# Optimization experiments

Hardware: AMD Instinct MI355X
Metric: run time of the kernel (lower is better)

## Reference

```python
import jax, jax.numpy as jnp
import numpy as np

B, S, E = 2, 2048, 1024
H, D = 16, 64  # num_heads, head_dim


def setup_inputs() -> dict:
    key = jax.random.key(0)
    k1, k2, k3 = jax.random.split(key, 3)
    x = jax.random.normal(k1, (B, S, E), dtype=jnp.float32)
    # nnx normal() init has stddev 0.01; scale to keep magnitudes realistic
    w_qkv = jax.random.normal(k2, (E, H, 3 * D), dtype=jnp.float32) * 0.01
    w_out = jax.random.normal(k3, (H, D, E), dtype=jnp.float32) * 0.01
    return {"x": x, "w_qkv": w_qkv, "w_out": w_out}


def _attention(q, k, v):
    # q,k,v: [B, S, H, D]
    dtype = q.dtype
    logits = jnp.einsum('bqhd,bkhd->bhqk', q.astype(jnp.float32), k.astype(jnp.float32))
    logits = logits / jnp.sqrt(jnp.float32(q.shape[-1]))
    mask = jnp.tril(jnp.ones((q.shape[1], q.shape[1]), dtype=jnp.bool_))
    neg = jnp.asarray(-0.7 * jnp.finfo(logits.dtype).max, dtype=logits.dtype)
    logits = jnp.where(mask, logits, neg)
    probs = jax.nn.softmax(logits, axis=-1).astype(dtype)
    return jnp.einsum('bhqk,bkhd->bqhd', probs, v)


def reference(x, w_qkv, w_out):
    # qkv projection: [B,S,E] x [E,H,3D] -> [B,S,H,3D]
    qkv = jnp.einsum('bse,ehd->bshd', x, w_qkv)
    q, k, v = jnp.split(qkv, 3, axis=-1)
    out = _attention(q, k, v)  # [B,S,H,D]
    # output projection contracts (H,D) -> E
    return jnp.einsum('bshd,hde->bse', out, w_out)
```

## Files before the change

### kernel.cpp

```cpp
#include <hip/hip_runtime.h>

typedef unsigned short u16;
typedef unsigned int u32;
typedef __attribute__((ext_vector_type(8))) short bf16x8;
typedef __attribute__((ext_vector_type(4))) float f32x4;
typedef __attribute__((ext_vector_type(16))) float f32x16;
typedef __attribute__((ext_vector_type(4))) u32 u32x4;

#define MFMA16(a, b, c) __builtin_amdgcn_mfma_f32_16x16x32_bf16((a), (b), (c), 0, 0, 0)
#define MFMA32(a, b, c) __builtin_amdgcn_mfma_f32_32x32x16_bf16((a), (b), (c), 0, 0, 0)

__device__ __forceinline__ void async_lds16(void* lds, const void* g) {
  __builtin_amdgcn_global_load_lds(
      (const __attribute__((address_space(1))) void*)g,
      (__attribute__((address_space(3))) void*)lds, 16, 0, 0);
}

__device__ __forceinline__ u16 f2bf(float f) {
  union { float f; unsigned u; } v; v.f = f;
  unsigned r = v.u + 0x7fffu + ((v.u >> 16) & 1u);
  return (u16)(r >> 16);
}

__device__ __forceinline__ u32 cvt_pk_bf16(float lo, float hi) {
  u32 r;
  asm("v_cvt_pk_bf16_f32 %0, %1, %2" : "=v"(r) : "v"(lo), "v"(hi));
  return r;
}

__device__ __forceinline__ float exp2_fast(float x) {
  float r;
  asm("v_exp_f32 %0, %1" : "=v"(r) : "v"(x));
  return r;
}

__device__ __forceinline__ void pswap(u32& a, u32& b) {
  asm("v_permlane32_swap_b32 %0, %1" : "+v"(a), "+v"(b));
}


__global__ __launch_bounds__(256) void k_cvt(const float* __restrict__ in, u16* __restrict__ out, int n) {
  int i = (blockIdx.x * 256 + threadIdx.x) * 4;
  if (i >= n) return;
  float4 v = *(const float4*)(in + i);
  ushort4 o;
  o.x = f2bf(v.x); o.y = f2bf(v.y); o.z = f2bf(v.z); o.w = f2bf(v.w);
  *(ushort4*)(out + i) = o;
}

__global__ __launch_bounds__(256) void k_transpose_cvt(const float* __restrict__ in, u16* __restrict__ out,
                                                       int R, int C) {
  __shared__ float tile[32][33];
  int c0 = blockIdx.x * 32, r0 = blockIdx.y * 32;
  int tx = threadIdx.x & 31, ty = threadIdx.x >> 5;
#pragma unroll
  for (int i = 0; i < 32; i += 8)
    tile[ty + i][tx] = in[(long)(r0 + ty + i) * C + c0 + tx];
  __syncthreads();
#pragma unroll
  for (int i = 0; i < 32; i += 8)
    out[(long)(c0 + ty + i) * R + r0 + tx] = f2bf(tile[tx][ty + i]);
}

__global__ __launch_bounds__(256) void k_transpose_v(const u16* __restrict__ V, u16* __restrict__ Vt) {
  int bh = blockIdx.z;
  int s0 = blockIdx.x * 32, d0 = blockIdx.y * 32;
  __shared__ u16 tile[32][33];
  int tx = threadIdx.x & 31, ty = threadIdx.x >> 5;
  const u16* Vb = V + (long)bh * 2048 * 64;
  u16* Vtb = Vt + (long)bh * 64 * 2048;
#pragma unroll
  for (int i = 0; i < 32; i += 8)
    tile[ty + i][tx] = Vb[(long)(s0 + ty + i) * 64 + d0 + tx];
  __syncthreads();
#pragma unroll
  for (int i = 0; i < 32; i += 8)
    Vtb[(long)(d0 + ty + i) * 2048 + s0 + tx] = tile[tx][ty + i];
}


template <int BM, int BN, int NW, int WN, int MR, int NR>
__device__ __forceinline__ void gemm_core_pipe(const u16* __restrict__ A, const u16* __restrict__ Bt,
                                               int K, long row0, long col0,
                                               u16* sA, u16* sB, f32x4 (&acc)[MR][NR]) {
  const int NTHR = NW * 64;
  const int ABYTES = BM * 64 * 2;
  const int BBYTES = BN * 64 * 2;
  const int t = threadIdx.x;
  const int lane = t & 63, g = lane >> 4, m16 = lane & 15;
  const int wid = t >> 6, wr = wid / WN, wc = wid % WN;
  const int nkt = K >> 6;

  auto stage = [&](int buf, int kt) {
    const int k0 = kt << 6;
#pragma unroll
    for (int it = 0; it < ABYTES / (NTHR * 16); ++it) {
      int i = it * NTHR + t;
      int r = i >> 3, c = i & 7, cs = c ^ (r & 7);
      async_lds16((char*)sA + buf * ABYTES + i * 16, A + (row0 + r) * K + k0 + cs * 8);
    }
#pragma unroll
    for (int it = 0; it < BBYTES / (NTHR * 16); ++it) {
      int i = it * NTHR + t;
      int r = i >> 3, c = i & 7, cs = c ^ (r & 7);
      async_lds16((char*)sB + buf * BBYTES + i * 16, Bt + (col0 + r) * K + k0 + cs * 8);
    }
  };

  stage(0, 0);
  stage(1, 1);
  int cur = 0;
  for (int kt = 0; kt < nkt; ++kt) {
    if (kt + 1 < nkt) asm volatile("s_waitcnt vmcnt(8)" ::: "memory");
    else              asm volatile("s_waitcnt vmcnt(0)" ::: "memory");
    __builtin_amdgcn_s_barrier();
    __builtin_amdgcn_sched_barrier(0);
    const char* bA = (const char*)sA + cur * ABYTES;
    const char* bB = (const char*)sB + cur * BBYTES;
#pragma unroll
    for (int kk6 = 0; kk6 < 2; ++kk6) {
      const int ke = kk6 * 32 + 8 * g;
      bf16x8 av[MR], bv[NR];
#pragma unroll
      for (int mi = 0; mi < MR; ++mi) {
        int row = wr * (MR * 16) + mi * 16 + m16;
        av[mi] = *(const bf16x8*)(bA + (row << 7) + ((ke << 1) ^ ((row & 7) << 4)));
      }
#pragma unroll
      for (int ni = 0; ni < NR; ++ni) {
        int row = wc * (NR * 16) + ni * 16 + m16;
        bv[ni] = *(const bf16x8*)(bB + (row << 7) + ((ke << 1) ^ ((row & 7) << 4)));
      }
#pragma unroll
      for (int mi = 0; mi < MR; ++mi)
#pragma unroll
        for (int ni = 0; ni < NR; ++ni)
          acc[mi][ni] = MFMA16(av[mi], bv[ni], acc[mi][ni]);
    }
    __builtin_amdgcn_sched_barrier(0);
    __builtin_amdgcn_s_barrier();
    if (kt + 2 < nkt) stage(cur, kt + 2);
    cur ^= 1;
  }
}

__global__ __launch_bounds__(512, 2) void k_gemm_qkv(const u16* __restrict__ xb, const u16* __restrict__ wT,
                                                     u16* __restrict__ Qo, u16* __restrict__ Ko,
                                                     u16* __restrict__ Vo) {
  __shared__ __align__(16) u16 sA[2 * 256 * 64];
  __shared__ __align__(16) u16 sB[2 * 256 * 64];
  f32x4 acc[8][4];
  const f32x4 z = {0.f, 0.f, 0.f, 0.f};
#pragma unroll
  for (int mi = 0; mi < 8; ++mi)
#pragma unroll
    for (int ni = 0; ni < 4; ++ni) acc[mi][ni] = z;
  const int L = blockIdx.x;
  const int xcd = L & 7, idx = L >> 3;
  const int rowt = xcd * 2 + (idx & 1);
  const int colt = idx >> 1;
  long row0 = (long)rowt * 256, col0 = (long)colt * 256;
  gemm_core_pipe<256, 256, 8, 4, 8, 4>(xb, wT, 1024, row0, col0, sA, sB, acc);
  const int t = threadIdx.x;
  const int lane = t & 63, g = lane >> 4, m16 = lane & 15;
  const int wid = t >> 6, wr = wid >> 2, wc = wid & 3;
#pragma unroll
  for (int mi = 0; mi < 8; ++mi) {
#pragma unroll
    for (int ni = 0; ni < 4; ++ni) {
      int col = (int)col0 + wc * 64 + ni * 16 + m16;
      int h = col / 192, rem = col - h * 192;
      int which = rem >> 6, d = rem & 63;
#pragma unroll
      for (int r = 0; r < 4; ++r) {
        int row = (int)row0 + wr * 128 + mi * 16 + 4 * g + r;
        int b = row >> 11, s = row & 2047;
        long off = (((long)(b * 16 + h)) * 2048 + s) * 64 + d;
        float v = acc[mi][ni][r];
        if (which == 0) Qo[off] = f2bf(v * 0.18033688f);
        else if (which == 1) Ko[off] = f2bf(v);
        else Vo[off] = f2bf(v);
      }
    }
  }
}

__global__ __launch_bounds__(256) void k_gemm_out(const u16* __restrict__ Ob, const u16* __restrict__ wT,
                                                  float* __restrict__ out) {
  __shared__ __align__(16) u16 sA[2 * 128 * 64];
  __shared__ __align__(16) u16 sB[2 * 128 * 64];
  f32x4 acc[4][4];
  const f32x4 z = {0.f, 0.f, 0.f, 0.f};
#pragma unroll
  for (int mi = 0; mi < 4; ++mi)
#pragma unroll
    for (int ni = 0; ni < 4; ++ni) acc[mi][ni] = z;
  const int L = blockIdx.x;
  const int xcd = L & 7, idx = L >> 3;
  const int rowt = xcd * 4 + (idx & 3);
  const int colt = idx >> 2;
  long row0 = (long)rowt * 128, col0 = (long)colt * 128;
  gemm_core_pipe<128, 128, 4, 2, 4, 4>(Ob, wT, 1024, row0, col0, sA, sB, acc);
  const int t = threadIdx.x;
  const int lane = t & 63, g = lane >> 4, m16 = lane & 15;
  const int wid = t >> 6, wr = wid >> 1, wc = wid & 1;
#pragma unroll
  for (int mi = 0; mi < 4; ++mi) {
#pragma unroll
    for (int ni = 0; ni < 4; ++ni) {
#pragma unroll
      for (int r = 0; r < 4; ++r) {
        long row = row0 + wr * 64 + mi * 16 + 4 * g + r;
        long col = col0 + wc * 64 + ni * 16 + m16;
        out[row * 1024 + col] = acc[mi][ni][r];
      }
    }
  }
}


template <bool DIAG>
__device__ __forceinline__ void attn_sub(const char* Kt, const char* Vt, int bsub,
                                         bf16x8 qf0, bf16x8 qf1, bf16x8 qf2, bf16x8 qf3,
                                         f32x16& acc0, f32x16& acc1, float& l,
                                         int q5, int hi) {
  const int x7 = q5 & 7;
  const int rowK = (bsub * 32 + q5) << 7;
  bf16x8 k0 = *(const bf16x8*)(Kt + rowK + (((0 + hi) ^ x7) << 4));
  bf16x8 k1 = *(const bf16x8*)(Kt + rowK + (((2 + hi) ^ x7) << 4));
  bf16x8 k2 = *(const bf16x8*)(Kt + rowK + (((4 + hi) ^ x7) << 4));
  bf16x8 k3 = *(const bf16x8*)(Kt + rowK + (((6 + hi) ^ x7) << 4));
  const int rowV0 = q5 << 7, rowV1 = (q5 + 32) << 7;
  bf16x8 v00 = *(const bf16x8*)(Vt + rowV0 + (((bsub * 4 + 0 + hi) ^ x7) << 4));
  bf16x8 v01 = *(const bf16x8*)(Vt + rowV1 + (((bsub * 4 + 0 + hi) ^ x7) << 4));
  bf16x8 v10 = *(const bf16x8*)(Vt + rowV0 + (((bsub * 4 + 2 + hi) ^ x7) << 4));
  bf16x8 v11 = *(const bf16x8*)(Vt + rowV1 + (((bsub * 4 + 2 + hi) ^ x7) << 4));

  f32x16 s;
#pragma unroll
  for (int r = 0; r < 16; ++r) s[r] = 0.f;
  s = MFMA32(k0, qf0, s);
  s = MFMA32(k1, qf1, s);
  s = MFMA32(k2, qf2, s);
  s = MFMA32(k3, qf3, s);

  float p[16];
#pragma unroll
  for (int r = 0; r < 16; ++r) {
    float pv = exp2_fast(s[r]);
    if (DIAG) {
      int crow = (r & 3) + 8 * (r >> 2) + 4 * hi;
      pv = (crow <= q5) ? pv : 0.f;
    }
    p[r] = pv;
  }
  l += (((p[0] + p[1]) + (p[2] + p[3])) + ((p[4] + p[5]) + (p[6] + p[7]))) +
       (((p[8] + p[9]) + (p[10] + p[11])) + ((p[12] + p[13]) + (p[14] + p[15])));

  u32 a0 = cvt_pk_bf16(p[0], p[1]), a1 = cvt_pk_bf16(p[2], p[3]);
  u32 b0 = cvt_pk_bf16(p[4], p[5]), b1 = cvt_pk_bf16(p[6], p[7]);
  pswap(a0, b0); pswap(a1, b1);
  u32 c0 = cvt_pk_bf16(p[8], p[9]), c1 = cvt_pk_bf16(p[10], p[11]);
  u32 d0 = cvt_pk_bf16(p[12], p[13]), d1 = cvt_pk_bf16(p[14], p[15]);
  pswap(c0, d0); pswap(c1, d1);
  u32x4 t0; t0[0] = a0; t0[1] = a1; t0[2] = b0; t0[3] = b1;
  u32x4 t1; t1[0] = c0; t1[1] = c1; t1[2] = d0; t1[3] = d1;
  bf16x8 pa0 = __builtin_bit_cast(bf16x8, t0);
  bf16x8 pa1 = __builtin_bit_cast(bf16x8, t1);

  acc0 = MFMA32(pa0, v00, acc0);
  acc1 = MFMA32(pa0, v01, acc1);
  acc0 = MFMA32(pa1, v10, acc0);
  acc1 = MFMA32(pa1, v11, acc1);
}

__global__ __launch_bounds__(256) void k_attn(const u16* __restrict__ Qg, const u16* __restrict__ Kg,
                                              const u16* __restrict__ Vtg, u16* __restrict__ Og) {
  __shared__ __align__(16) u16 sK[2][64 * 64];
  __shared__ __align__(16) u16 sV[2][64 * 64];
  const int t = threadIdx.x;
  const int lane = t & 63, q5 = lane & 31, hi = lane >> 5, w = t >> 6;
  const int L = blockIdx.x;
  const int bh = L & 31, pr = L >> 5;
  const int qtA = pr, qtB = 15 - pr;
  const int b = bh >> 4, h = bh & 15;
  const u16* Qh = Qg + (long)bh * 131072;
  const u16* Kh = Kg + (long)bh * 131072;
  const u16* Vh = Vtg + (long)bh * 131072;
  char* sKb = (char*)sK;
  char* sVb = (char*)sV;

  const int sL_ = qtA * 4 + w, sH_ = qtB * 4 + w;
  const int q0L = sL_ * 32, q0H = sH_ * 32;
  const int nkt = 2 * qtB + 2;

  const u16* QpL = Qh + (long)(q0L + q5) * 64 + hi * 8;
  bf16x8 qfL0 = *(const bf16x8*)(QpL);
  bf16x8 qfL1 = *(const bf16x8*)(QpL + 16);
  bf16x8 qfL2 = *(const bf16x8*)(QpL + 32);
  bf16x8 qfL3 = *(const bf16x8*)(QpL + 48);
  const u16* QpH = Qh + (long)(q0H + q5) * 64 + hi * 8;
  bf16x8 qfH0 = *(const bf16x8*)(QpH);
  bf16x8 qfH1 = *(const bf16x8*)(QpH + 16);
  bf16x8 qfH2 = *(const bf16x8*)(QpH + 32);
  bf16x8 qfH3 = *(const bf16x8*)(QpH + 48);

  f32x16 aL0, aL1, aH0, aH1;
#pragma unroll
  for (int r = 0; r < 16; ++r) { aL0[r] = 0.f; aL1[r] = 0.f; aH0[r] = 0.f; aH1[r] = 0.f; }
  float lL = 0.f, lH = 0.f;

  auto stage = [&](int buf, int kt) {
    const int kbase = kt << 6;
#pragma unroll
    for (int ps = 0; ps < 2; ++ps) {
      int i = ps * 256 + t;
      int r = i >> 3, c = i & 7, cs = c ^ (r & 7);
      async_lds16(sKb + buf * 8192 + i * 16, Kh + (long)(kbase + r) * 64 + cs * 8);
    }
#pragma unroll
    for (int ps = 0; ps < 2; ++ps) {
      int i = ps * 256 + t;
      int d = i >> 3, c = i & 7, cs = c ^ (d & 7);
      async_lds16(sVb + buf * 8192 + i * 16, Vh + (long)d * 2048 + kbase + cs * 8);
    }
  };

  stage(0, 0);
  stage(1, 1);
  int cur = 0;
#pragma unroll 1
  for (int kt = 0; kt < nkt; ++kt) {
    if (kt + 1 < nkt) asm volatile("s_waitcnt vmcnt(4)" ::: "memory");
    else              asm volatile("s_waitcnt vmcnt(0)" ::: "memory");
    __builtin_amdgcn_s_barrier();
    __builtin_amdgcn_sched_barrier(0);
    const char* Kt = sKb + cur * 8192;
    const char* Vt = sVb + cur * 8192;
    const int c2 = 2 * kt;
    if (c2 <= sH_) {
      if (c2 == sH_) attn_sub<true>(Kt, Vt, 0, qfH0, qfH1, qfH2, qfH3, aH0, aH1, lH, q5, hi);
      else           attn_sub<false>(Kt, Vt, 0, qfH0, qfH1, qfH2, qfH3, aH0, aH1, lH, q5, hi);
    }
    if (c2 + 1 <= sH_) {
      if (c2 + 1 == sH_) attn_sub<true>(Kt, Vt, 1, qfH0, qfH1, qfH2, qfH3, aH0, aH1, lH, q5, hi);
      else               attn_sub<false>(Kt, Vt, 1, qfH0, qfH1, qfH2, qfH3, aH0, aH1, lH, q5, hi);
    }
    if (c2 <= sL_) {
      if (c2 == sL_) attn_sub<true>(Kt, Vt, 0, qfL0, qfL1, qfL2, qfL3, aL0, aL1, lL, q5, hi);
      else           attn_sub<false>(Kt, Vt, 0, qfL0, qfL1, qfL2, qfL3, aL0, aL1, lL, q5, hi);
    }
    if (c2 + 1 <= sL_) {
      if (c2 + 1 == sL_) attn_sub<true>(Kt, Vt, 1, qfL0, qfL1, qfL2, qfL3, aL0, aL1, lL, q5, hi);
      else               attn_sub<false>(Kt, Vt, 1, qfL0, qfL1, qfL2, qfL3, aL0, aL1, lL, q5, hi);
    }
    __builtin_amdgcn_sched_barrier(0);
    __builtin_amdgcn_s_barrier();
    if (kt + 2 < nkt) stage(cur, kt + 2);
    cur ^= 1;
  }

  const long orow_base = (long)b * 2048;
  lH += __shfl_xor(lH, 32);
  float liH = 1.0f / lH;
#pragma unroll
  for (int r = 0; r < 16; ++r) {
    int crow = (r & 3) + 8 * (r >> 2) + 4 * hi;
    float lf = __shfl(liH, crow);
    long orow = orow_base + q0H + crow;
    Og[orow * 1024 + h * 64 + q5] = f2bf(aH0[r] * lf);
    Og[orow * 1024 + h * 64 + 32 + q5] = f2bf(aH1[r] * lf);
  }
  lL += __shfl_xor(lL, 32);
  float liL = 1.0f / lL;
#pragma unroll
  for (int r = 0; r < 16; ++r) {
    int crow = (r & 3) + 8 * (r >> 2) + 4 * hi;
    float lf = __shfl(liL, crow);
    long orow = orow_base + q0L + crow;
    Og[orow * 1024 + h * 64 + q5] = f2bf(aL0[r] * lf);
    Og[orow * 1024 + h * 64 + 32 + q5] = f2bf(aL1[r] * lf);
  }
}


extern "C" void kernel_launch(void* const* d_in, const int* in_sizes, int n_in,
                              void* d_out, int out_size, void* d_ws, size_t ws_size,
                              hipStream_t stream) {
  const float* x = (const float*)d_in[0];
  const float* w_qkv = (const float*)d_in[1];
  const float* w_out = (const float*)d_in[2];
  float* out = (float*)d_out;
  char* ws = (char*)d_ws;

  u16* xb    = (u16*)(ws + 0);
  u16* wqkvT = (u16*)(ws + 8388608L);
  u16* woutT = (u16*)(ws + 14680064L);
  u16* Qb    = (u16*)(ws + 16777216L);
  u16* Kb    = (u16*)(ws + 25165824L);
  u16* Vb    = (u16*)(ws + 33554432L);
  u16* Vt    = (u16*)(ws + 41943040L);
  u16* Ob    = xb;

  k_cvt<<<4096, 256, 0, stream>>>(x, xb, 4194304);
  k_transpose_cvt<<<dim3(96, 32), 256, 0, stream>>>(w_qkv, wqkvT, 1024, 3072);
  k_transpose_cvt<<<dim3(32, 32), 256, 0, stream>>>(w_out, woutT, 1024, 1024);
  k_gemm_qkv<<<dim3(192), 512, 0, stream>>>(xb, wqkvT, Qb, Kb, Vb);
  k_transpose_v<<<dim3(64, 2, 32), 256, 0, stream>>>(Vb, Vt);
  k_attn<<<dim3(256), 256, 0, stream>>>(Qb, Kb, Vt, Ob);
  k_gemm_out<<<dim3(256), 256, 0, stream>>>(Ob, woutT, out);
}
```

Measured before the change: 122.5 us.

## Merge prep kernels, retile QKV GEMM to per-head 192 columns, raise MFMA priority

Three launches (x conversion and two weight transpose-converts) become one k_prep kernel that dispatches on block index, removing two launch gaps. The QKV GEMM tile changes from 256x256 to 256x192, so each column tile covers exactly one head, giving 256 blocks instead of 192 and simpler epilogue index math. The vmcnt wait is adjusted to the new load count. Attention MFMA sections are wrapped in s_setprio to favour the matrix issue; the smaller tile slightly lowers reuse per block.

Measured after the change: 113.3 us. -7.5%, faster.

```diff
diff --git a/kernel.cpp b/kernel.cpp
--- a/kernel.cpp
+++ b/kernel.cpp
@@ -39,19 +39,10 @@
 }
 
 
-__global__ __launch_bounds__(256) void k_cvt(const float* __restrict__ in, u16* __restrict__ out, int n) {
-  int i = (blockIdx.x * 256 + threadIdx.x) * 4;
-  if (i >= n) return;
-  float4 v = *(const float4*)(in + i);
-  ushort4 o;
-  o.x = f2bf(v.x); o.y = f2bf(v.y); o.z = f2bf(v.z); o.w = f2bf(v.w);
-  *(ushort4*)(out + i) = o;
-}
-
-__global__ __launch_bounds__(256) void k_transpose_cvt(const float* __restrict__ in, u16* __restrict__ out,
-                                                       int R, int C) {
-  __shared__ float tile[32][33];
-  int c0 = blockIdx.x * 32, r0 = blockIdx.y * 32;
+__device__ __forceinline__ void transpose_cvt_body(const float* __restrict__ in, u16* __restrict__ out,
+                                                   int R, int C, int bx, int by,
+                                                   float (*tile)[33]) {
+  int c0 = bx * 32, r0 = by * 32;
   int tx = threadIdx.x & 31, ty = threadIdx.x >> 5;
 #pragma unroll
   for (int i = 0; i < 32; i += 8)
@@ -60,6 +51,26 @@
 #pragma unroll
   for (int i = 0; i < 32; i += 8)
     out[(long)(c0 + ty + i) * R + r0 + tx] = f2bf(tile[tx][ty + i]);
+}
+
+__global__ __launch_bounds__(256) void k_prep(const float* __restrict__ x, u16* __restrict__ xb,
+                                              const float* __restrict__ w_qkv, u16* __restrict__ wqkvT,
+                                              const float* __restrict__ w_out, u16* __restrict__ woutT) {
+  __shared__ float tile[32][33];
+  const int B = blockIdx.x;
+  if (B < 4096) {
+    int i = (B * 256 + threadIdx.x) * 4;
+    float4 v = *(const float4*)(x + i);
+    ushort4 o;
+    o.x = f2bf(v.x); o.y = f2bf(v.y); o.z = f2bf(v.z); o.w = f2bf(v.w);
+    *(ushort4*)(xb + i) = o;
+  } else if (B < 7168) {
+    int bb = B - 4096;
+    transpose_cvt_body(w_qkv, wqkvT, 1024, 3072, bb % 96, bb / 96, tile);
+  } else {
+    int bb = B - 7168;
+    transpose_cvt_body(w_out, woutT, 1024, 1024, bb & 31, bb >> 5, tile);
+  }
 }
 
 __global__ __launch_bounds__(256) void k_transpose_v(const u16* __restrict__ V, u16* __restrict__ Vt) {
@@ -79,7 +90,7 @@
 }
 
 
-template <int BM, int BN, int NW, int WN, int MR, int NR>
+template <int BM, int BN, int NW, int WN, int WCS, int MR, int NR, int NLD>
 __device__ __forceinline__ void gemm_core_pipe(const u16* __restrict__ A, const u16* __restrict__ Bt,
                                                int K, long row0, long col0,
                                                u16* sA, u16* sB, f32x4 (&acc)[MR][NR]) {
@@ -111,8 +122,12 @@
   stage(1, 1);
   int cur = 0;
   for (int kt = 0; kt < nkt; ++kt) {
-    if (kt + 1 < nkt) asm volatile("s_waitcnt vmcnt(8)" ::: "memory");
-    else              asm volatile("s_waitcnt vmcnt(0)" ::: "memory");
+    if (kt + 1 < nkt) {
+      if constexpr (NLD == 7) asm volatile("s_waitcnt vmcnt(7)" ::: "memory");
+      else                    asm volatile("s_waitcnt vmcnt(8)" ::: "memory");
+    } else {
+      asm volatile("s_waitcnt vmcnt(0)" ::: "memory");
+    }
     __builtin_amdgcn_s_barrier();
     __builtin_amdgcn_sched_barrier(0);
     const char* bA = (const char*)sA + cur * ABYTES;
@@ -128,7 +143,7 @@
       }
 #pragma unroll
       for (int ni = 0; ni < NR; ++ni) {
-        int row = wc * (NR * 16) + ni * 16 + m16;
+        int row = wc * WCS + ni * 16 + m16;
         bv[ni] = *(const bf16x8*)(bB + (row << 7) + ((ke << 1) ^ ((row & 7) << 4)));
       }
 #pragma unroll
@@ -148,28 +163,28 @@
                                                      u16* __restrict__ Qo, u16* __restrict__ Ko,
                                                      u16* __restrict__ Vo) {
   __shared__ __align__(16) u16 sA[2 * 256 * 64];
-  __shared__ __align__(16) u16 sB[2 * 256 * 64];
-  f32x4 acc[8][4];
+  __shared__ __align__(16) u16 sB[2 * 192 * 64];
+  f32x4 acc[8][3];
   const f32x4 z = {0.f, 0.f, 0.f, 0.f};
 #pragma unroll
   for (int mi = 0; mi < 8; ++mi)
 #pragma unroll
-    for (int ni = 0; ni < 4; ++ni) acc[mi][ni] = z;
+    for (int ni = 0; ni < 3; ++ni) acc[mi][ni] = z;
   const int L = blockIdx.x;
   const int xcd = L & 7, idx = L >> 3;
   const int rowt = xcd * 2 + (idx & 1);
   const int colt = idx >> 1;
-  long row0 = (long)rowt * 256, col0 = (long)colt * 256;
-  gemm_core_pipe<256, 256, 8, 4, 8, 4>(xb, wT, 1024, row0, col0, sA, sB, acc);
+  long row0 = (long)rowt * 256, col0 = (long)colt * 192;
+  gemm_core_pipe<256, 192, 8, 4, 48, 8, 3, 7>(xb, wT, 1024, row0, col0, sA, sB, acc);
   const int t = threadIdx.x;
   const int lane = t & 63, g = lane >> 4, m16 = lane & 15;
   const int wid = t >> 6, wr = wid >> 2, wc = wid & 3;
+  const int h = colt;
 #pragma unroll
   for (int mi = 0; mi < 8; ++mi) {
 #pragma unroll
-    for (int ni = 0; ni < 4; ++ni) {
-      int col = (int)col0 + wc * 64 + ni * 16 + m16;
-      int h = col / 192, rem = col - h * 192;
+    for (int ni = 0; ni < 3; ++ni) {
+      int rem = wc * 48 + ni * 16 + m16;
       int which = rem >> 6, d = rem & 63;
 #pragma unroll
       for (int r = 0; r < 4; ++r) {
@@ -200,7 +215,7 @@
   const int rowt = xcd * 4 + (idx & 3);
   const int colt = idx >> 2;
   long row0 = (long)rowt * 128, col0 = (long)colt * 128;
-  gemm_core_pipe<128, 128, 4, 2, 4, 4>(Ob, wT, 1024, row0, col0, sA, sB, acc);
+  gemm_core_pipe<128, 128, 4, 2, 64, 4, 4, 8>(Ob, wT, 1024, row0, col0, sA, sB, acc);
   const int t = threadIdx.x;
   const int lane = t & 63, g = lane >> 4, m16 = lane & 15;
   const int wid = t >> 6, wr = wid >> 1, wc = wid & 1;
@@ -239,10 +254,12 @@
   f32x16 s;
 #pragma unroll
   for (int r = 0; r < 16; ++r) s[r] = 0.f;
+  __builtin_amdgcn_s_setprio(1);
   s = MFMA32(k0, qf0, s);
   s = MFMA32(k1, qf1, s);
   s = MFMA32(k2, qf2, s);
   s = MFMA32(k3, qf3, s);
+  __builtin_amdgcn_s_setprio(0);
 
   float p[16];
 #pragma unroll
@@ -268,10 +285,12 @@
   bf16x8 pa0 = __builtin_bit_cast(bf16x8, t0);
   bf16x8 pa1 = __builtin_bit_cast(bf16x8, t1);
 
+  __builtin_amdgcn_s_setprio(1);
   acc0 = MFMA32(pa0, v00, acc0);
   acc1 = MFMA32(pa0, v01, acc1);
   acc0 = MFMA32(pa1, v10, acc0);
   acc1 = MFMA32(pa1, v11, acc1);
+  __builtin_amdgcn_s_setprio(0);
 }
 
 __global__ __launch_bounds__(256) void k_attn(const u16* __restrict__ Qg, const u16* __restrict__ Kg,
@@ -402,10 +421,8 @@
   u16* Vt    = (u16*)(ws + 41943040L);
   u16* Ob    = xb;
 
-  k_cvt<<<4096, 256, 0, stream>>>(x, xb, 4194304);
-  k_transpose_cvt<<<dim3(96, 32), 256, 0, stream>>>(w_qkv, wqkvT, 1024, 3072);
-  k_transpose_cvt<<<dim3(32, 32), 256, 0, stream>>>(w_out, woutT, 1024, 1024);
-  k_gemm_qkv<<<dim3(192), 512, 0, stream>>>(xb, wqkvT, Qb, Kb, Vb);
+  k_prep<<<dim3(8192), 256, 0, stream>>>(x, xb, w_qkv, wqkvT, w_out, woutT);
+  k_gemm_qkv<<<dim3(256), 512, 0, stream>>>(xb, wqkvT, Qb, Kb, Vb);
   k_transpose_v<<<dim3(64, 2, 32), 256, 0, stream>>>(Vb, Vt);
   k_attn<<<dim3(256), 256, 0, stream>>>(Qb, Kb, Vt, Ob);
   k_gemm_out<<<dim3(256), 256, 0, stream>>>(Ob, woutT, out);
```
